# Kernel optimization log

Hardware: AMD Instinct MI355X
Metric: run time of the kernel (lower is better)

The kernel has to match this reference:

```python
import jax, jax.numpy as jnp
import numpy as np

EMBED_DIM = 1152
NUM_HEADS = 16
PROJ_SIZE = 1152
HEAD_DIM = PROJ_SIZE // NUM_HEADS  # 72
SEQ = 16384
N_SEG = 8
SEG_LEN = SEQ // N_SEG


def setup_inputs() -> dict:
    key = jax.random.key(0)
    ks = jax.random.split(key, 6)
    hidden_states = jax.random.normal(ks[0], (1, SEQ, EMBED_DIM), dtype=jnp.float32)
    qkv_w = jax.random.normal(ks[1], (3 * PROJ_SIZE, EMBED_DIM), dtype=jnp.float32) * 0.02
    qkv_b = jax.random.normal(ks[2], (3 * PROJ_SIZE,), dtype=jnp.float32) * 0.02
    out_w = jax.random.normal(ks[3], (EMBED_DIM, PROJ_SIZE), dtype=jnp.float32) * 0.02
    out_b = jax.random.normal(ks[4], (EMBED_DIM,), dtype=jnp.float32) * 0.02
    # rotary frequencies (seq, head_dim/2), full-head-dim rotary since 2*36 == 72
    rotary_pos_emb = jax.random.uniform(ks[5], (SEQ, HEAD_DIM // 2), dtype=jnp.float32) * 6.2831853
    cu_seqlens = jnp.arange(N_SEG + 1, dtype=jnp.int32) * SEG_LEN
    return {
        "hidden_states": hidden_states,
        "qkv_w": qkv_w,
        "qkv_b": qkv_b,
        "out_w": out_w,
        "out_b": out_b,
        "rotary_pos_emb": rotary_pos_emb,
        "cu_seqlens": cu_seqlens,
    }


def _rotate_half(x):
    x1, x2 = jnp.split(x, 2, axis=-1)
    return jnp.concatenate([-x2, x1], axis=-1)


def _apply_rope(x, cos, sin):
    # x: (b, s, h, d); cos/sin: (s, d) broadcast over batch and heads
    cos = cos[None, :, None, :]
    sin = sin[None, :, None, :]
    return x * cos + _rotate_half(x) * sin


def _forward(hidden_states, qkv_w, qkv_b, out_w, out_b, rotary_pos_emb, cu):
    b, s, _ = hidden_states.shape
    x = jnp.swapaxes(hidden_states, 0, 1)          # (s, b, embed)
    qkv = x @ qkv_w.T + qkv_b                      # (s, b, 3*proj)
    q, k, v = jnp.split(qkv, 3, axis=-1)
    def to_bshd(t):
        t = t.reshape(s, b, NUM_HEADS, HEAD_DIM)
        return jnp.swapaxes(t, 0, 1)               # (b, s, h, d)
    q, k, v = to_bshd(q), to_bshd(k), to_bshd(v)

    # rotary: cos/sin (s, d/2) -> (s, d) via non-interleaved repeat '(2 d)'
    cos = jnp.cos(rotary_pos_emb)
    sin = jnp.sin(rotary_pos_emb)
    cos2 = jnp.concatenate([cos, cos], axis=-1)    # (s, d)
    sin2 = jnp.concatenate([sin, sin], axis=-1)
    q = _apply_rope(q, cos2, sin2)
    k = _apply_rope(k, cos2, sin2)

    # block-diagonal (varlen) attention per cu_seqlens segment
    scale = 1.0 / np.sqrt(HEAD_DIM)
    outs = []
    for i in range(len(cu) - 1):
        s0, s1 = int(cu[i]), int(cu[i + 1])
        qi, ki, vi = q[:, s0:s1], k[:, s0:s1], v[:, s0:s1]   # (b, L, h, d)
        scores = jnp.einsum('bqhd,bkhd->bhqk', qi, ki) * scale
        attn = jax.nn.softmax(scores, axis=-1)
        outs.append(jnp.einsum('bhqk,bkhd->bqhd', attn, vi))
    ctx = jnp.concatenate(outs, axis=1)            # (b, s, h, d)
    ctx = jnp.swapaxes(ctx, 0, 1).reshape(s, b, PROJ_SIZE)  # (s, b, proj)
    out = ctx @ out_w.T + out_b                    # (s, b, embed)
    return jnp.swapaxes(out, 0, 1)                 # (b, s, embed)


def reference(hidden_states, qkv_w, qkv_b, out_w, out_b, rotary_pos_emb, cu_seqlens):
    cu = np.asarray(cu_seqlens)  # static segment boundaries
    return _forward(hidden_states, qkv_w, qkv_b, out_w, out_b, rotary_pos_emb, cu)
```

## Files before the change

### kernel.cpp

```cpp
#include <hip/hip_runtime.h>
#include <hip/hip_bf16.h>
#include <cstdint>

#define SEQ   16384
#define ED    1152
#define NH    16
#define HD    72
#define NSEG  8
#define SEGLEN 2048
#define QKVN  3456
#define NT    (SEGLEN / 64)
#define VTROWS 80

typedef __bf16 bf16x8 __attribute__((ext_vector_type(8)));
typedef float  f32x4  __attribute__((ext_vector_type(4)));
typedef __hip_bfloat16 bf16;

__device__ __forceinline__ unsigned short f2bfbits(float f) {
  bf16 h = __float2bfloat16(f);
  return __builtin_bit_cast(unsigned short, h);
}

__device__ __forceinline__ float fexp2(float x) {
#if __has_builtin(__builtin_amdgcn_exp2f)
  return __builtin_amdgcn_exp2f(x);
#else
  return exp2f(x);
#endif
}

__device__ __forceinline__ unsigned short f2bf_rhu(float f) {
  unsigned int b = __builtin_bit_cast(unsigned int, f);
  return (unsigned short)((b + 0x8000u) >> 16);
}

__device__ __forceinline__ void gload_lds16(const void* g, void* l) {
  __builtin_amdgcn_global_load_lds(
      (__attribute__((address_space(1))) void*)(void*)g,
      (__attribute__((address_space(3))) void*)l, 16, 0, 0);
}

__global__ __launch_bounds__(256) void cvt_f32_bf16(const float* __restrict__ in,
                                                    bf16* __restrict__ out, int n4) {
  int i = blockIdx.x * 256 + threadIdx.x;
  if (i >= n4) return;
  float4 v = reinterpret_cast<const float4*>(in)[i];
  ushort4 o;
  o.x = f2bfbits(v.x); o.y = f2bfbits(v.y); o.z = f2bfbits(v.z); o.w = f2bfbits(v.w);
  reinterpret_cast<ushort4*>(out)[i] = o;
}

__global__ __launch_bounds__(256) void gemm_bt(const bf16* __restrict__ A,
                                               const bf16* __restrict__ B,
                                               const float* __restrict__ bias,
                                               void* __restrict__ Cout,
                                               int M, int N, int K, int out_bf16) {
  __shared__ __align__(16) bf16 As[2 * 128 * 32];
  __shared__ __align__(16) bf16 Bs[2 * 128 * 32];
  const int nt   = N >> 7;
  const int nwg  = gridDim.x;
  const int cpx  = nwg >> 3;
  const int bid  = blockIdx.x;
  const int swz  = (bid & 7) * cpx + (bid >> 3);
  const int bm   = swz / nt;
  const int bn   = swz % nt;
  const int tid  = threadIdx.x;
  const int lane = tid & 63;
  const int wave = tid >> 6;
  const int wr   = wave >> 1, wc = wave & 1;

  const bf16* Ab = A + (size_t)(bm * 128) * K;
  const bf16* Bb = B + (size_t)(bn * 128) * K;

  char* AsB = (char*)As;
  char* BsB = (char*)Bs;

  const int row15 = lane & 15;
  const int koff  = (lane >> 4) << 3;
  const int srow  = lane >> 2;
  const int scol  = (lane & 3) << 3;

  f32x4 acc[4][4] = {};

  for (int k0 = 0; k0 < K; k0 += 64) {
#pragma unroll
    for (int i = wave; i < 16; i += 4) {
      const int kk = i >> 3, ib = i & 7;
      gload_lds16(Ab + (size_t)(ib * 16 + srow) * K + k0 + kk * 32 + scol, AsB + i * 1024);
      gload_lds16(Bb + (size_t)(ib * 16 + srow) * K + k0 + kk * 32 + scol, BsB + i * 1024);
    }
    __syncthreads();
#pragma unroll
    for (int kk = 0; kk < 2; ++kk) {
      bf16x8 a[4], b[4];
#pragma unroll
      for (int mi = 0; mi < 4; ++mi)
        a[mi] = *reinterpret_cast<const bf16x8*>(&As[kk * 4096 + (wr * 64 + mi * 16 + row15) * 32 + koff]);
#pragma unroll
      for (int ni = 0; ni < 4; ++ni)
        b[ni] = *reinterpret_cast<const bf16x8*>(&Bs[kk * 4096 + (wc * 64 + ni * 16 + row15) * 32 + koff]);
#pragma unroll
      for (int mi = 0; mi < 4; ++mi)
#pragma unroll
        for (int ni = 0; ni < 4; ++ni)
          acc[mi][ni] = __builtin_amdgcn_mfma_f32_16x16x32_bf16(a[mi], b[ni], acc[mi][ni], 0, 0, 0);
    }
    __syncthreads();
  }

  const int crow = bm * 128 + wr * 64 + (lane >> 4) * 4;
  const int ccol = bn * 128 + wc * 64 + row15;
#pragma unroll
  for (int mi = 0; mi < 4; ++mi)
#pragma unroll
    for (int ni = 0; ni < 4; ++ni) {
      const int col = ccol + ni * 16;
      const float bv = bias[col];
#pragma unroll
      for (int r = 0; r < 4; ++r) {
        const int row = crow + mi * 16 + r;
        float v = acc[mi][ni][r] + bv;
        if (out_bf16)
          reinterpret_cast<bf16*>(Cout)[(size_t)row * N + col] = __float2bfloat16(v);
        else
          reinterpret_cast<float*>(Cout)[(size_t)row * N + col] = v;
      }
    }
}

__global__ __launch_bounds__(256) void rope_inplace(bf16* __restrict__ qkv,
                                                    const float* __restrict__ ang) {
  const int s = blockIdx.x;
  bf16* row = qkv + (size_t)s * QKVN;
  for (int i = threadIdx.x; i < 2 * NH * 36; i += 256) {
    int t   = i / (NH * 36);
    int rem = i - t * (NH * 36);
    int h   = rem / 36;
    int d2  = rem - h * 36;
    float a  = ang[s * 36 + d2];
    float cs = cosf(a), sn = sinf(a);
    bf16* p = row + t * ED + h * HD + d2;
    float x1 = __bfloat162float(p[0]);
    float x2 = __bfloat162float(p[36]);
    p[0]  = __float2bfloat16(x1 * cs - x2 * sn);
    p[36] = __float2bfloat16(x2 * cs + x1 * sn);
  }
}

__global__ __launch_bounds__(256, 4) void transpose_v(const bf16* __restrict__ qkv,
                                                      bf16* __restrict__ vt) {
  const int h  = blockIdx.x & 15;
  const int st = blockIdx.x >> 4;
  const int s0 = st * 64;
  const int tid = threadIdx.x;
  __shared__ __align__(16) bf16 Lt[72 * 72];

  const bf16* src = qkv + (size_t)s0 * QKVN + 2 * ED + h * HD;
  for (int c = tid; c < 576; c += 256) {
    int j = c / 9, m9 = c - j * 9;
    int d0 = m9 << 3;
    int jj = (j + (m9 << 3)) & 63;
    bf16x8 v = *reinterpret_cast<const bf16x8*>(src + (size_t)j * QKVN + d0);
    const unsigned short* u = reinterpret_cast<const unsigned short*>(&v);
#pragma unroll
    for (int e = 0; e < 8; ++e)
      Lt[(d0 + e) * 72 + jj] = __builtin_bit_cast(bf16, u[e]);
  }
  __syncthreads();

  bf16x8 ones8, zero8 = {};
  {
    unsigned short ob = f2bfbits(1.0f);
#pragma unroll
    for (int e = 0; e < 8; ++e) ones8[e] = __builtin_bit_cast(__bf16, ob);
  }
  bf16* dst = vt + (size_t)(h * VTROWS) * SEQ + s0;
  for (int c = tid; c < VTROWS * 8; c += 256) {
    int d = c >> 3, sc = c & 7;
    bf16x8 v;
    int og = sc;
    if (d < 72) {
      int col = (((sc + (d >> 3)) << 3)) & 63;
      v = *reinterpret_cast<const bf16x8*>(&Lt[d * 72 + col]);
      og = (sc + (d & 7)) & 7;
    } else {
      v = (d == 72) ? ones8 : zero8;
    }
    *reinterpret_cast<bf16x8*>(dst + (size_t)d * SEQ + (og << 3)) = v;
  }
}

__global__ __launch_bounds__(512, 4) void attn(const bf16* __restrict__ qkv,
                                               const bf16* __restrict__ vt,
                                               bf16* __restrict__ ctx) {
  const int blk  = blockIdx.x;
  const int qt   = (blk >> 3) & 7;
  const int g    = (((blk >> 6) & 15) << 3) | (blk & 7);
  const int head = g & 15;
  const int seg  = g >> 4;
  const int q0   = seg * SEGLEN + qt * 256;

  const int tid = threadIdx.x, lane = tid & 63, w = tid >> 6;
  const int row15 = lane & 15, hi = lane >> 4, koff = hi << 3;

  __shared__ __align__(16) bf16 Ks[64 * 72];
  __shared__ __align__(16) bf16 Vt[VTROWS * 64];
  __shared__ __align__(16) bf16 Ps[256 * 72];

  const bf16* Qg  = qkv + (size_t)q0 * QKVN + head * HD;
  const bf16* Kg  = qkv + (size_t)(seg * SEGLEN) * QKVN + ED + head * HD;
  const bf16* Vtg = vt + (size_t)(head * VTROWS) * SEQ + seg * SEGLEN;

  const bf16x8 zero8 = {};
  bf16x8 aq[2][3];
#pragma unroll
  for (int m = 0; m < 2; ++m) {
    const bf16* qrow = Qg + (size_t)(w * 32 + m * 16 + row15) * QKVN;
    aq[m][0] = *reinterpret_cast<const bf16x8*>(qrow + koff);
    aq[m][1] = *reinterpret_cast<const bf16x8*>(qrow + 32 + koff);
    aq[m][2] = (hi == 0) ? *reinterpret_cast<const bf16x8*>(qrow + 64) : zero8;
  }

  f32x4 oacc[2][5] = {};
  const float c2 = 0.11785113019775793f * 1.4426950408889634f;

  auto stage_k = [&](int kt2) {
    const bf16* Kt = Kg + (size_t)kt2 * 64 * QKVN;
    char* KsB = (char*)Ks;
    for (int gq = w; gq < 9; gq += 8) {
      int chunk = gq * 64 + lane;
      int row = chunk / 9;
      int cc  = chunk - row * 9;
      gload_lds16(Kt + (size_t)row * QKVN + cc * 8, KsB + gq * 1024);
    }
  };

  auto stage_v = [&](int kt2) {
    const bf16* Vsrc = Vtg + (size_t)kt2 * 64;
    char* VsB = (char*)Vt;
    for (int i = w; i < 10; i += 8) {
      int c = i * 64 + lane;
      int d = c >> 3, g8 = c & 7;
      gload_lds16(Vsrc + (size_t)d * SEQ + g8 * 8, VsB + i * 1024);
    }
  };

  auto qkt_soft = [&]() {
    f32x4 s[2][4] = {};
    __builtin_amdgcn_s_setprio(1);
#pragma unroll
    for (int ks = 0; ks < 2; ++ks) {
#pragma unroll
      for (int n = 0; n < 4; ++n) {
        bf16x8 bk = *reinterpret_cast<const bf16x8*>(&Ks[(n * 16 + row15) * 72 + ks * 32 + koff]);
        s[0][n] = __builtin_amdgcn_mfma_f32_16x16x32_bf16(aq[0][ks], bk, s[0][n], 0, 0, 0);
        s[1][n] = __builtin_amdgcn_mfma_f32_16x16x32_bf16(aq[1][ks], bk, s[1][n], 0, 0, 0);
      }
    }
#pragma unroll
    for (int n = 0; n < 4; ++n) {
      bf16x8 bk = (hi == 0) ? *reinterpret_cast<const bf16x8*>(&Ks[(n * 16 + row15) * 72 + 64]) : zero8;
      s[0][n] = __builtin_amdgcn_mfma_f32_16x16x32_bf16(aq[0][2], bk, s[0][n], 0, 0, 0);
      s[1][n] = __builtin_amdgcn_mfma_f32_16x16x32_bf16(aq[1][2], bk, s[1][n], 0, 0, 0);
    }
    __builtin_amdgcn_s_setprio(0);
    const int prow_base = w * 32 + hi * 4;
#pragma unroll
    for (int m = 0; m < 2; ++m)
#pragma unroll
      for (int n = 0; n < 4; ++n)
#pragma unroll
        for (int r = 0; r < 4; ++r) {
          float p = fexp2(fmaf(s[m][n][r], c2, -4.0f));
          Ps[(prow_base + m * 16 + r) * 72 + n * 16 + row15] =
              __builtin_bit_cast(bf16, f2bf_rhu(p));
        }
  };

  auto pv = [&]() {
    __builtin_amdgcn_s_setprio(1);
#pragma unroll
    for (int ks = 0; ks < 2; ++ks) {
      bf16x8 ap0 = *reinterpret_cast<const bf16x8*>(&Ps[(w * 32 + row15) * 72 + ks * 32 + koff]);
      bf16x8 ap1 = *reinterpret_cast<const bf16x8*>(&Ps[(w * 32 + 16 + row15) * 72 + ks * 32 + koff]);
#pragma unroll
      for (int n = 0; n < 5; ++n) {
        const int vrow = n * 16 + row15;
        const int cA = ((((ks << 2) + hi + (vrow & 7)) & 7) << 3);
        bf16x8 bv = *reinterpret_cast<const bf16x8*>(&Vt[vrow * 64 + cA]);
        oacc[0][n] = __builtin_amdgcn_mfma_f32_16x16x32_bf16(ap0, bv, oacc[0][n], 0, 0, 0);
        oacc[1][n] = __builtin_amdgcn_mfma_f32_16x16x32_bf16(ap1, bv, oacc[1][n], 0, 0, 0);
      }
    }
    __builtin_amdgcn_s_setprio(0);
  };

  stage_k(0);
  stage_v(0);
  for (int kt = 0; kt < NT; ++kt) {
    __syncthreads();
    qkt_soft();
    pv();
    __syncthreads();
    if (kt + 1 < NT) {
      stage_k(kt + 1);
      stage_v(kt + 1);
    }
  }

#pragma unroll
  for (int m = 0; m < 2; ++m) {
#pragma unroll
    for (int r = 0; r < 4; ++r) {
      float l = __shfl(oacc[m][4][r], (lane & 48) + 8);
      float inv = 1.0f / l;
#pragma unroll
      for (int n = 0; n < 5; ++n) {
        const int d = n * 16 + row15;
        if (d < HD) {
          const int row = q0 + w * 32 + m * 16 + hi * 4 + r;
          ctx[(size_t)row * ED + head * HD + d] = __float2bfloat16(oacc[m][n][r] * inv);
        }
      }
    }
  }
}

extern "C" void kernel_launch(void* const* d_in, const int* in_sizes, int n_in,
                              void* d_out, int out_size, void* d_ws, size_t ws_size,
                              hipStream_t stream) {
  const float* hidden = (const float*)d_in[0];
  const float* qkv_w  = (const float*)d_in[1];
  const float* qkv_b  = (const float*)d_in[2];
  const float* out_w  = (const float*)d_in[3];
  const float* out_b  = (const float*)d_in[4];
  const float* rope   = (const float*)d_in[5];

  const size_t SZ_QKV = (size_t)SEQ * QKVN * 2;
  const size_t SZ_X   = (size_t)SEQ * ED * 2;
  const size_t SZ_W   = (size_t)QKVN * ED * 2;
  const size_t SZ_VT  = (size_t)NH * VTROWS * SEQ * 2;
  const size_t NEED   = SZ_QKV + SZ_X + SZ_W + SZ_VT;
  if (ws_size < NEED) return;

  char* ws = (char*)d_ws;
  bf16* qkvbf = (bf16*)(ws);
  bf16* Xbf   = (bf16*)(ws + SZ_QKV);
  bf16* Wbf   = (bf16*)(ws + SZ_QKV + SZ_X);
  bf16* vtb   = (bf16*)(ws + SZ_QKV + SZ_X + SZ_W);

  cvt_f32_bf16<<<(SEQ * ED / 4 + 255) / 256, 256, 0, stream>>>(hidden, Xbf, SEQ * ED / 4);
  cvt_f32_bf16<<<(QKVN * ED / 4 + 255) / 256, 256, 0, stream>>>(qkv_w, Wbf, QKVN * ED / 4);

  gemm_bt<<<(SEQ / 128) * (QKVN / 128), 256, 0, stream>>>(Xbf, Wbf, qkv_b, qkvbf,
                                                          SEQ, QKVN, ED, 1);

  cvt_f32_bf16<<<(ED * ED / 4 + 255) / 256, 256, 0, stream>>>(out_w, Wbf, ED * ED / 4);

  rope_inplace<<<SEQ, 256, 0, stream>>>(qkvbf, rope);

  transpose_v<<<NH * (SEQ / 64), 256, 0, stream>>>(qkvbf, vtb);

  attn<<<NSEG * NH * (SEGLEN / 256), 512, 0, stream>>>(qkvbf, vtb, Xbf);

  gemm_bt<<<(SEQ / 128) * (ED / 128), 256, 0, stream>>>(Xbf, Wbf, out_b, d_out,
                                                        SEQ, ED, ED, 0);
}
```

Before: 517.5 us.

## Double-buffer K and V tiles in LDS to overlap loads with compute

Splits the shared-memory K and V tiles into two buffers selected by tile parity. The next tile's async global-to-LDS loads are issued before the current tile's QK^T/softmax and PV MFMAs, and one of the two per-iteration barriers is removed. The aim is to hide global load latency behind matrix work and cut barrier stalls. In exchange, LDS use per block grows by about 19 KB, which could limit how many blocks fit on a CU.

```diff
diff --git a/kernel.cpp b/kernel.cpp
--- a/kernel.cpp
+++ b/kernel.cpp
@@ -11,6 +11,8 @@
 #define QKVN  3456
 #define NT    (SEGLEN / 64)
 #define VTROWS 80
+#define KSZ   (64 * 72)
+#define VSZ   (VTROWS * 64)
 
 typedef __bf16 bf16x8 __attribute__((ext_vector_type(8)));
 typedef float  f32x4  __attribute__((ext_vector_type(4)));
@@ -203,8 +205,8 @@
   const int tid = threadIdx.x, lane = tid & 63, w = tid >> 6;
   const int row15 = lane & 15, hi = lane >> 4, koff = hi << 3;
 
-  __shared__ __align__(16) bf16 Ks[64 * 72];
-  __shared__ __align__(16) bf16 Vt[VTROWS * 64];
+  __shared__ __align__(16) bf16 Ks[2 * KSZ];
+  __shared__ __align__(16) bf16 Vt[2 * VSZ];
   __shared__ __align__(16) bf16 Ps[256 * 72];
 
   const bf16* Qg  = qkv + (size_t)q0 * QKVN + head * HD;
@@ -226,7 +228,7 @@
 
   auto stage_k = [&](int kt2) {
     const bf16* Kt = Kg + (size_t)kt2 * 64 * QKVN;
-    char* KsB = (char*)Ks;
+    char* KsB = (char*)(Ks + (kt2 & 1) * KSZ);
     for (int gq = w; gq < 9; gq += 8) {
       int chunk = gq * 64 + lane;
       int row = chunk / 9;
@@ -237,7 +239,7 @@
 
   auto stage_v = [&](int kt2) {
     const bf16* Vsrc = Vtg + (size_t)kt2 * 64;
-    char* VsB = (char*)Vt;
+    char* VsB = (char*)(Vt + (kt2 & 1) * VSZ);
     for (int i = w; i < 10; i += 8) {
       int c = i * 64 + lane;
       int d = c >> 3, g8 = c & 7;
@@ -245,21 +247,22 @@
     }
   };
 
-  auto qkt_soft = [&]() {
+  auto qkt_soft = [&](int sel) {
+    const bf16* ks = Ks + sel * KSZ;
     f32x4 s[2][4] = {};
     __builtin_amdgcn_s_setprio(1);
 #pragma unroll
-    for (int ks = 0; ks < 2; ++ks) {
+    for (int kc = 0; kc < 2; ++kc) {
 #pragma unroll
       for (int n = 0; n < 4; ++n) {
-        bf16x8 bk = *reinterpret_cast<const bf16x8*>(&Ks[(n * 16 + row15) * 72 + ks * 32 + koff]);
-        s[0][n] = __builtin_amdgcn_mfma_f32_16x16x32_bf16(aq[0][ks], bk, s[0][n], 0, 0, 0);
-        s[1][n] = __builtin_amdgcn_mfma_f32_16x16x32_bf16(aq[1][ks], bk, s[1][n], 0, 0, 0);
+        bf16x8 bk = *reinterpret_cast<const bf16x8*>(&ks[(n * 16 + row15) * 72 + kc * 32 + koff]);
+        s[0][n] = __builtin_amdgcn_mfma_f32_16x16x32_bf16(aq[0][kc], bk, s[0][n], 0, 0, 0);
+        s[1][n] = __builtin_amdgcn_mfma_f32_16x16x32_bf16(aq[1][kc], bk, s[1][n], 0, 0, 0);
       }
     }
 #pragma unroll
     for (int n = 0; n < 4; ++n) {
-      bf16x8 bk = (hi == 0) ? *reinterpret_cast<const bf16x8*>(&Ks[(n * 16 + row15) * 72 + 64]) : zero8;
+      bf16x8 bk = (hi == 0) ? *reinterpret_cast<const bf16x8*>(&ks[(n * 16 + row15) * 72 + 64]) : zero8;
       s[0][n] = __builtin_amdgcn_mfma_f32_16x16x32_bf16(aq[0][2], bk, s[0][n], 0, 0, 0);
       s[1][n] = __builtin_amdgcn_mfma_f32_16x16x32_bf16(aq[1][2], bk, s[1][n], 0, 0, 0);
     }
@@ -277,17 +280,18 @@
         }
   };
 
-  auto pv = [&]() {
+  auto pv = [&](int sel) {
+    const bf16* vb = Vt + sel * VSZ;
     __builtin_amdgcn_s_setprio(1);
 #pragma unroll
-    for (int ks = 0; ks < 2; ++ks) {
-      bf16x8 ap0 = *reinterpret_cast<const bf16x8*>(&Ps[(w * 32 + row15) * 72 + ks * 32 + koff]);
-      bf16x8 ap1 = *reinterpret_cast<const bf16x8*>(&Ps[(w * 32 + 16 + row15) * 72 + ks * 32 + koff]);
+    for (int ks2 = 0; ks2 < 2; ++ks2) {
+      bf16x8 ap0 = *reinterpret_cast<const bf16x8*>(&Ps[(w * 32 + row15) * 72 + ks2 * 32 + koff]);
+      bf16x8 ap1 = *reinterpret_cast<const bf16x8*>(&Ps[(w * 32 + 16 + row15) * 72 + ks2 * 32 + koff]);
 #pragma unroll
       for (int n = 0; n < 5; ++n) {
         const int vrow = n * 16 + row15;
-        const int cA = ((((ks << 2) + hi + (vrow & 7)) & 7) << 3);
-        bf16x8 bv = *reinterpret_cast<const bf16x8*>(&Vt[vrow * 64 + cA]);
+        const int cA = ((((ks2 << 2) + hi + (vrow & 7)) & 7) << 3);
+        bf16x8 bv = *reinterpret_cast<const bf16x8*>(&vb[vrow * 64 + cA]);
         oacc[0][n] = __builtin_amdgcn_mfma_f32_16x16x32_bf16(ap0, bv, oacc[0][n], 0, 0, 0);
         oacc[1][n] = __builtin_amdgcn_mfma_f32_16x16x32_bf16(ap1, bv, oacc[1][n], 0, 0, 0);
       }
@@ -299,13 +303,12 @@
   stage_v(0);
   for (int kt = 0; kt < NT; ++kt) {
     __syncthreads();
-    qkt_soft();
-    pv();
-    __syncthreads();
     if (kt + 1 < NT) {
       stage_k(kt + 1);
       stage_v(kt + 1);
     }
+    qkt_soft(kt & 1);
+    pv(kt & 1);
   }
 
 #pragma unroll
```

Measured after the change: 516.3 us. About the same (-0.2%).
